# Kernel tuning notes

Measured on AMD Instinct MI355X. Metric: run time of the kernel, lower is better.

Reference implementation:

```python
import jax, jax.numpy as jnp
import numpy as np

B, S, D, H = 4, 2048, 1024, 16
DH = D // H
NEG = -100000.0


def setup_inputs() -> dict:
    key = jax.random.key(0)
    ks = jax.random.split(key, 13)
    s = 1.0 / np.sqrt(D)
    inp = {
        'q': jax.random.normal(ks[0], (B, S, D), jnp.float32),
        'k': jax.random.normal(ks[1], (B, S, D), jnp.float32),
        'v': jax.random.normal(ks[2], (B, S, D), jnp.float32),
        'mask': jax.random.randint(ks[3], (B, 1, S, S), 0, 2).astype(bool),
        'wq_w': jax.random.normal(ks[4], (D, D), jnp.float32) * s,
        'wq_b': jnp.zeros((D,), jnp.float32),
        'wk_w': jax.random.normal(ks[5], (D, D), jnp.float32) * s,
        'wk_b': jnp.zeros((D,), jnp.float32),
        'wv_w': jax.random.normal(ks[6], (D, D), jnp.float32) * s,
        'wv_b': jnp.zeros((D,), jnp.float32),
        'wo_w': jax.random.normal(ks[7], (D, D), jnp.float32) * s,
        'wo_b': jnp.zeros((D,), jnp.float32),
    }
    return inp


def reference(q, k, v, mask, wq_w, wq_b, wk_w, wk_b, wv_w, wv_b, wo_w, wo_b):
    # torch Linear: y = x @ W^T + b
    qh = (q @ wq_w.T + wq_b).reshape(B, S, H, DH).transpose(0, 2, 1, 3)  # [B,H,S,DH]
    kh = (k @ wk_w.T + wk_b).reshape(B, S, H, DH).transpose(0, 2, 1, 3)
    vh = (v @ wv_w.T + wv_b).reshape(B, S, H, DH).transpose(0, 2, 1, 3)
    # NOTE: original code has NO 1/sqrt(d) scaling
    alpha = jnp.einsum('bhqd,bhkd->bhqk', qh, kh)  # [B,H,S,S]
    alpha = jnp.where(mask, NEG, alpha)
    score = jax.nn.softmax(alpha, axis=-1)
    x = jnp.einsum('bhqk,bhkd->bhqd', score, vh)
    x = x.transpose(0, 2, 1, 3).reshape(B, S, D)
    return x @ wo_w.T + wo_b
```

## Files before the change

kernel.cpp:

```cpp
#include <hip/hip_runtime.h>
#include <hip/hip_bf16.h>

#define B_ 4
#define S_ 2048
#define D_ 1024
#define H_ 16
#define NEGV (-100000.0f)

typedef __attribute__((ext_vector_type(8))) short short8;
typedef __attribute__((ext_vector_type(4))) float f32x4;
typedef unsigned short us;

__device__ __forceinline__ us f2h(float f) {
  union { _Float16 h; us u; } c;
  c.h = (_Float16)f;
  return c.u;
}

__global__ void detect_mask_kernel(const int* __restrict__ mi, int* __restrict__ flag) {
  int t = threadIdx.x;
  bool bad = false;
  for (int i = t; i < 16384; i += 64) {
    int v = mi[i];
    bad = bad || (v != 0 && v != 1);
  }
  unsigned long long any = __ballot(bad);
  if (t == 0) flag[0] = (any != 0ull) ? 1 : 0;
}

__global__ __launch_bounds__(256) void pack_mask(const void* __restrict__ maskp,
                                                 const int* __restrict__ flag,
                                                 unsigned* __restrict__ pk) {
  int w = blockIdx.x * 256 + threadIdx.x;
  unsigned bits = 0;
  if (flag[0]) {
    const uint4* p = (const uint4*)((const unsigned char*)maskp + (size_t)w * 32);
#pragma unroll
    for (int q = 0; q < 2; ++q) {
      uint4 v = p[q];
      unsigned vv[4] = {v.x, v.y, v.z, v.w};
#pragma unroll
      for (int e = 0; e < 4; ++e) {
        unsigned byte4 = vv[e];
#pragma unroll
        for (int bb = 0; bb < 4; ++bb)
          bits |= (unsigned)(((byte4 >> (8 * bb)) & 0xffu) != 0) << (q * 16 + e * 4 + bb);
      }
    }
  } else {
    const uint4* p = (const uint4*)((const int*)maskp + (size_t)w * 32);
#pragma unroll
    for (int q = 0; q < 8; ++q) {
      uint4 v = p[q];
      bits |= (unsigned)(v.x != 0) << (q * 4 + 0);
      bits |= (unsigned)(v.y != 0) << (q * 4 + 1);
      bits |= (unsigned)(v.z != 0) << (q * 4 + 2);
      bits |= (unsigned)(v.w != 0) << (q * 4 + 3);
    }
  }
  pk[w] = bits;
}

__global__ __launch_bounds__(256) void cvt_f16(const float* __restrict__ in,
                                               us* __restrict__ out, int n8) {
  int i = blockIdx.x * 256 + threadIdx.x;
  if (i >= n8) return;
  float4 a = ((const float4*)in)[2 * i];
  float4 b = ((const float4*)in)[2 * i + 1];
  us u[8] = {f2h(a.x), f2h(a.y), f2h(a.z), f2h(a.w),
             f2h(b.x), f2h(b.y), f2h(b.z), f2h(b.w)};
  ((uint4*)out)[i] = *(uint4*)u;
}

__global__ __launch_bounds__(256) void cvt_w4(const float* __restrict__ w0,
                                              const float* __restrict__ w1,
                                              const float* __restrict__ w2,
                                              const float* __restrict__ w3,
                                              us* __restrict__ d0, us* __restrict__ d1,
                                              us* __restrict__ d2, us* __restrict__ d3) {
  int which = blockIdx.x >> 9;
  int i = (blockIdx.x & 511) * 256 + threadIdx.x;
  const float* w = which == 0 ? w0 : which == 1 ? w1 : which == 2 ? w2 : w3;
  us* d = which == 0 ? d0 : which == 1 ? d1 : which == 2 ? d2 : d3;
  float4 a = ((const float4*)w)[2 * i];
  float4 b = ((const float4*)w)[2 * i + 1];
  us u[8] = {f2h(a.x), f2h(a.y), f2h(a.z), f2h(a.w),
             f2h(b.x), f2h(b.y), f2h(b.z), f2h(b.w)};
  ((uint4*)d)[i] = *(uint4*)u;
}

__device__ __forceinline__ void gload16(const us* g, us* l) {
  __builtin_amdgcn_global_load_lds((const __attribute__((address_space(1))) void*)g,
                                   (__attribute__((address_space(3))) void*)l, 16, 0, 0);
}

__device__ __forceinline__ int swzb(int row, int c16) {
  return row * 128 + ((c16 ^ (row & 7)) << 4);
}

template <int OMODE>
__global__ __launch_bounds__(256) void gemm_mfma(
    const us* __restrict__ A, const us* __restrict__ W,
    const float* __restrict__ bias, void* __restrict__ Cp, int M, int N, int K) {
  __shared__ __align__(16) us As[2][128 * 64];
  __shared__ __align__(16) us Ws[2][128 * 64];

  const int m0 = blockIdx.x * 128;
  const int n0 = blockIdx.y * 128;
  const int t = threadIdx.x;
  const int w = t >> 6, l = t & 63;
  const int l15 = l & 15, l4 = l >> 4;
  const int wm = w >> 1, wn = w & 1;

  int goff[4];
#pragma unroll
  for (int j = 0; j < 4; ++j) {
    int u = t + j * 256;
    int r = u >> 3, c8 = u & 7;
    int g = c8 ^ (r & 7);
    goff[j] = r * K + g * 8;
  }
  const us* Ag = A + (size_t)m0 * K;
  const us* Wg = W + (size_t)n0 * K;

  f32x4 acc[4][4];
#pragma unroll
  for (int m = 0; m < 4; ++m)
#pragma unroll
    for (int n = 0; n < 4; ++n) acc[m][n] = (f32x4){0.f, 0.f, 0.f, 0.f};

  auto stage = [&](int k0, int bb) {
#pragma unroll
    for (int j = 0; j < 4; ++j) {
      int u = t + j * 256;
      gload16(Ag + goff[j] + k0, &As[bb][u * 8]);
      gload16(Wg + goff[j] + k0, &Ws[bb][u * 8]);
    }
  };

  stage(0, 0);
  __syncthreads();
  int cur = 0;
  for (int k0 = 0; k0 < K; k0 += 64) {
    if (k0 + 64 < K) stage(k0 + 64, cur ^ 1);
#pragma unroll
    for (int ks = 0; ks < 2; ++ks) {
      short8 ah[4], bh_[4];
#pragma unroll
      for (int m = 0; m < 4; ++m)
        ah[m] = *(const short8*)((const char*)As[cur] + swzb(wm * 64 + m * 16 + l15, ks * 4 + l4));
#pragma unroll
      for (int n = 0; n < 4; ++n)
        bh_[n] = *(const short8*)((const char*)Ws[cur] + swzb(wn * 64 + n * 16 + l15, ks * 4 + l4));
#pragma unroll
      for (int m = 0; m < 4; ++m)
#pragma unroll
        for (int n = 0; n < 4; ++n)
          acc[m][n] = __builtin_amdgcn_mfma_f32_16x16x32_f16(ah[m], bh_[n], acc[m][n], 0, 0, 0);
    }
    __syncthreads();
    cur ^= 1;
  }

  float bv[4];
#pragma unroll
  for (int n = 0; n < 4; ++n) bv[n] = bias[n0 + wn * 64 + n * 16 + l15];

#pragma unroll
  for (int m = 0; m < 4; ++m) {
#pragma unroll
    for (int i = 0; i < 4; ++i) {
      int gm = m0 + wm * 64 + m * 16 + l4 * 4 + i;
#pragma unroll
      for (int n = 0; n < 4; ++n) {
        int gn = n0 + wn * 64 + n * 16 + l15;
        float o = acc[m][n][i] + bv[n];
        if constexpr (OMODE == 0) {
          ((float*)Cp)[(size_t)gm * N + gn] = o;
        } else {
          int b = gm >> 11, s = gm & (S_ - 1);
          int hh = gn >> 6, d = gn & 63;
          size_t idx = (((size_t)(b * H_ + hh) << 11) + s) * 64 + d;
          ((us*)Cp)[idx] = f2h(o);
        }
      }
    }
  }
}

__global__ __launch_bounds__(256) void transpose_v(const us* __restrict__ vh,
                                                   us* __restrict__ vt) {
  __shared__ us Ts[64][72];
  int blk = blockIdx.x;
  int bh = blk >> 5, s0 = (blk & 31) << 6;
  int t = threadIdx.x;
#pragma unroll
  for (int p = 0; p < 2; ++p) {
    int c = t + p * 256;
    int rs = c >> 3, c8 = c & 7;
    *(uint4*)&Ts[rs][c8 * 8] = *(const uint4*)(vh + ((size_t)bh * S_ + s0 + rs) * 64 + c8 * 8);
  }
  __syncthreads();
#pragma unroll
  for (int p = 0; p < 2; ++p) {
    int c = t + p * 256;
    int rd = c >> 3, s8 = c & 7;
    union { us u[8]; uint4 v; } tmp;
#pragma unroll
    for (int e = 0; e < 8; ++e) tmp.u[e] = Ts[s8 * 8 + e][rd];
    *(uint4*)(vt + ((size_t)bh * 64 + rd) * S_ + s0 + s8 * 8) = tmp.v;
  }
}

__device__ __forceinline__ int swz(int row, int bc) {
  return (row << 7) + (bc ^ ((row & 7) << 4));
}

__global__ __launch_bounds__(512) void attn_mfma(
    const us* __restrict__ qh, const us* __restrict__ kh,
    const us* __restrict__ vt, const unsigned* __restrict__ pk,
    us* __restrict__ xout) {
  __shared__ __align__(16) us Ks[2][4096];
  __shared__ __align__(16) us Vs[2][4096];
  __shared__ __align__(16) char Ps[16384];

  const int blk = ((blockIdx.x & 7) << 7) + (blockIdx.x >> 3);
  const int bh = blk >> 4;
  const int q0 = (blk & 15) << 7;
  const int b = bh >> 4, h = bh & (H_ - 1);
  const int t = threadIdx.x;
  const int w = t >> 6, l = t & 63;
  const int l15 = l & 15, l4 = l >> 4;

  short8 qf[2];
  {
    const size_t qbase = ((size_t)bh * S_ + q0 + 16 * w + l15) * 64 + l4 * 8;
    qf[0] = *(const short8*)(qh + qbase);
    qf[1] = *(const short8*)(qh + qbase + 32);
  }

  f32x4 accO[4];
#pragma unroll
  for (int jd = 0; jd < 4; ++jd) accO[jd] = (f32x4){0.f, 0.f, 0.f, 0.f};
  float m_i[4], l_p[4];
#pragma unroll
  for (int i = 0; i < 4; ++i) { m_i[i] = -1e30f; l_p[i] = 0.f; }

  const int r_st = t >> 3, c_st = (t & 7) ^ ((t >> 3) & 7);
  const us* kh_src = kh + ((size_t)bh * S_ + r_st) * 64 + c_st * 8;
  const us* vt_src = vt + ((size_t)bh * 64 + r_st) * S_ + c_st * 8;

  auto stage = [&](int k0, int bb) {
    gload16(kh_src + (size_t)k0 * 64, &Ks[bb][t * 8]);
    gload16(vt_src + k0, &Vs[bb][t * 8]);
  };

  stage(0, 0);
  __syncthreads();
  int cur = 0;
  const unsigned* pb = pk + ((size_t)b * S_ + q0 + 16 * w + (l4 << 2)) * (S_ / 32);

  for (int k0 = 0; k0 < S_; k0 += 64) {
    uint2 mw[4];
#pragma unroll
    for (int i = 0; i < 4; ++i) mw[i] = *(const uint2*)(pb + (size_t)i * (S_ / 32) + (k0 >> 5));
    if (k0 + 64 < S_) stage(k0 + 64, cur ^ 1);

    const char* KT = (const char*)Ks[cur];
    const char* VT = (const char*)Vs[cur];

    __builtin_amdgcn_s_setprio(1);
    f32x4 sj[4];
#pragma unroll
    for (int j = 0; j < 4; ++j) {
      f32x4 s = {0.f, 0.f, 0.f, 0.f};
#pragma unroll
      for (int c = 0; c < 2; ++c) {
        short8 kf = *(const short8*)(KT + swz(l15 + 16 * j, l4 * 16 + 64 * c));
        s = __builtin_amdgcn_mfma_f32_16x16x32_f16(qf[c], kf, s, 0, 0, 0);
      }
      sj[j] = s;
    }
    __builtin_amdgcn_s_setprio(0);
#pragma unroll
    for (int j = 0; j < 4; ++j) {
#pragma unroll
      for (int i = 0; i < 4; ++i) {
        unsigned bits = (j < 2) ? mw[i].x : mw[i].y;
        int sh = (l15 + 16 * j) & 31;
        if ((bits >> sh) & 1u) sj[j][i] = NEGV;
      }
    }
    float mx[4];
    bool need = false;
#pragma unroll
    for (int i = 0; i < 4; ++i) {
      float tm = fmaxf(fmaxf(sj[0][i], sj[1][i]), fmaxf(sj[2][i], sj[3][i]));
#pragma unroll
      for (int off = 1; off < 16; off <<= 1) tm = fmaxf(tm, __shfl_xor(tm, off));
      mx[i] = tm;
      need = need || (tm - m_i[i] > 8.0f);
    }
    if (__any(need)) {
#pragma unroll
      for (int i = 0; i < 4; ++i) {
        float mnew = fmaxf(m_i[i], mx[i]);
        float scl = __expf(m_i[i] - mnew);
        l_p[i] *= scl;
#pragma unroll
        for (int jd = 0; jd < 4; ++jd) accO[jd][i] *= scl;
        m_i[i] = mnew;
      }
    }
#pragma unroll
    for (int i = 0; i < 4; ++i) {
      int prow = 16 * w + l4 * 4 + i;
      float p0 = __expf(sj[0][i] - m_i[i]);
      float p1 = __expf(sj[1][i] - m_i[i]);
      float p2 = __expf(sj[2][i] - m_i[i]);
      float p3 = __expf(sj[3][i] - m_i[i]);
      l_p[i] += (p0 + p1) + (p2 + p3);
      unsigned pk01, pk23;
      asm("v_cvt_pkrtz_f16_f32 %0, %1, %2" : "=v"(pk01) : "v"(p0), "v"(p1));
      asm("v_cvt_pkrtz_f16_f32 %0, %1, %2" : "=v"(pk23) : "v"(p2), "v"(p3));
      *(us*)(Ps + swz(prow, l15 * 2)) = (us)pk01;
      *(us*)(Ps + swz(prow, (l15 + 16) * 2)) = (us)(pk01 >> 16);
      *(us*)(Ps + swz(prow, (l15 + 32) * 2)) = (us)pk23;
      *(us*)(Ps + swz(prow, (l15 + 48) * 2)) = (us)(pk23 >> 16);
    }
    asm volatile("s_waitcnt lgkmcnt(0)" ::: "memory");
    __builtin_amdgcn_sched_barrier(0);
    __builtin_amdgcn_s_setprio(1);
#pragma unroll
    for (int kc = 0; kc < 2; ++kc) {
      short8 pa = *(const short8*)(Ps + swz(16 * w + l15, l4 * 16 + 64 * kc));
#pragma unroll
      for (int jd = 0; jd < 4; ++jd) {
        short8 vb = *(const short8*)(VT + swz(l15 + 16 * jd, l4 * 16 + 64 * kc));
        accO[jd] = __builtin_amdgcn_mfma_f32_16x16x32_f16(pa, vb, accO[jd], 0, 0, 0);
      }
    }
    __builtin_amdgcn_s_setprio(0);
    __syncthreads();
    cur ^= 1;
  }

#pragma unroll
  for (int i = 0; i < 4; ++i) {
    float lr = l_p[i];
#pragma unroll
    for (int off = 1; off < 16; off <<= 1) lr += __shfl_xor(lr, off);
    float inv = 1.f / lr;
    int row = q0 + 16 * w + l4 * 4 + i;
    size_t obase = ((size_t)b * S_ + row) * D_ + h * 64 + l15;
#pragma unroll
    for (int jd = 0; jd < 4; ++jd) xout[obase + 16 * jd] = f2h(accO[jd][i] * inv);
  }
}

extern "C" void kernel_launch(void* const* d_in, const int* in_sizes, int n_in,
                              void* d_out, int out_size, void* d_ws, size_t ws_size,
                              hipStream_t stream) {
  const float* q = (const float*)d_in[0];
  const float* k = (const float*)d_in[1];
  const float* v = (const float*)d_in[2];
  const void* mask = d_in[3];
  const float* wq_w = (const float*)d_in[4];
  const float* wq_b = (const float*)d_in[5];
  const float* wk_w = (const float*)d_in[6];
  const float* wk_b = (const float*)d_in[7];
  const float* wv_w = (const float*)d_in[8];
  const float* wv_b = (const float*)d_in[9];
  const float* wo_w = (const float*)d_in[10];
  const float* wo_b = (const float*)d_in[11];

  const size_t NE = (size_t)B_ * S_ * D_;
  const size_t NW = (size_t)D_ * D_;
  char* ws = (char*)d_ws;
  int* flag = (int*)ws;
  unsigned* pk = (unsigned*)(ws + 256);
  us* C0 = (us*)(ws + 256 + (size_t)(B_ * S_ * (S_ / 32)) * 4);
  us* qh = C0 + NE;
  us* kh = qh + NE;
  us* vh = kh + NE;
  us* W0 = vh + NE;
  us* W1 = W0 + NW;
  us* W2 = W1 + NW;
  us* W3 = W2 + NW;

  detect_mask_kernel<<<1, 64, 0, stream>>>((const int*)mask, flag);
  pack_mask<<<(B_ * S_ * (S_ / 32)) / 256, 256, 0, stream>>>(mask, flag, pk);
  cvt_w4<<<2048, 256, 0, stream>>>(wq_w, wk_w, wv_w, wo_w, W0, W1, W2, W3);

  dim3 g(64, 8);
  const int n8 = (int)(NE / 8);

  cvt_f16<<<n8 / 256, 256, 0, stream>>>(q, C0, n8);
  gemm_mfma<2><<<g, 256, 0, stream>>>(C0, W0, wq_b, qh, B_ * S_, D_, D_);

  cvt_f16<<<n8 / 256, 256, 0, stream>>>(k, C0, n8);
  gemm_mfma<2><<<g, 256, 0, stream>>>(C0, W1, wk_b, kh, B_ * S_, D_, D_);

  cvt_f16<<<n8 / 256, 256, 0, stream>>>(v, C0, n8);
  gemm_mfma<2><<<g, 256, 0, stream>>>(C0, W2, wv_b, vh, B_ * S_, D_, D_);

  transpose_v<<<B_ * H_ * (S_ / 64), 256, 0, stream>>>(vh, C0);

  attn_mfma<<<B_ * H_ * (S_ / 128), 512, 0, stream>>>(qh, kh, C0, pk, vh);

  gemm_mfma<0><<<g, 256, 0, stream>>>(vh, W3, wo_b, d_out, B_ * S_, D_, D_);
}
```

Baseline: 404.4 us.

## Batch QKV projections into one launch and transpose S-tile MFMA in attention

The three input conversions and the three QKV projection GEMMs are merged into single launches using blockIdx.z, with a fallback path when workspace is too small. In the attention kernel the QK^T MFMA operands are swapped so each lane holds one query row. This lets softmax max and sum reductions use two cross-lane shuffles instead of per-row 16-lane reductions. Masking becomes branchless via fma, exp uses raw v_exp_f32 with log2e scaling, and P stores are widened to 64-bit. The batched GEMMs need more workspace, and the extra shuffles to rescale accumulator rows add some cost.

```diff
diff --git a/kernel.cpp b/kernel.cpp
--- a/kernel.cpp
+++ b/kernel.cpp
@@ -6,15 +6,22 @@
 #define D_ 1024
 #define H_ 16
 #define NEGV (-100000.0f)
+#define L2E 1.4426950408889634f
 
 typedef __attribute__((ext_vector_type(8))) short short8;
 typedef __attribute__((ext_vector_type(4))) float f32x4;
 typedef unsigned short us;
+typedef unsigned long long u64;
 
 __device__ __forceinline__ us f2h(float f) {
   union { _Float16 h; us u; } c;
   c.h = (_Float16)f;
   return c.u;
+}
+__device__ __forceinline__ float exp2a(float x) {
+  float r;
+  asm("v_exp_f32 %0, %1" : "=v"(r) : "v"(x));
+  return r;
 }
 
 __global__ void detect_mask_kernel(const int* __restrict__ mi, int* __restrict__ flag) {
@@ -61,10 +68,15 @@
   pk[w] = bits;
 }
 
-__global__ __launch_bounds__(256) void cvt_f16(const float* __restrict__ in,
-                                               us* __restrict__ out, int n8) {
-  int i = blockIdx.x * 256 + threadIdx.x;
-  if (i >= n8) return;
+__global__ __launch_bounds__(256) void cvt_f16x3(const float* __restrict__ i0,
+                                                 const float* __restrict__ i1,
+                                                 const float* __restrict__ i2,
+                                                 us* __restrict__ o0, us* __restrict__ o1,
+                                                 us* __restrict__ o2) {
+  int z = blockIdx.x >> 12;
+  int i = (blockIdx.x & 4095) * 256 + threadIdx.x;
+  const float* in = z == 0 ? i0 : z == 1 ? i1 : i2;
+  us* out = z == 0 ? o0 : z == 1 ? o1 : o2;
   float4 a = ((const float4*)in)[2 * i];
   float4 b = ((const float4*)in)[2 * i + 1];
   us u[8] = {f2h(a.x), f2h(a.y), f2h(a.z), f2h(a.w),
@@ -100,10 +112,19 @@
 
 template <int OMODE>
 __global__ __launch_bounds__(256) void gemm_mfma(
-    const us* __restrict__ A, const us* __restrict__ W,
-    const float* __restrict__ bias, void* __restrict__ Cp, int M, int N, int K) {
+    const us* __restrict__ A0, const us* __restrict__ A1, const us* __restrict__ A2,
+    const us* __restrict__ Wp0, const us* __restrict__ Wp1, const us* __restrict__ Wp2,
+    const float* __restrict__ b0, const float* __restrict__ b1, const float* __restrict__ b2,
+    void* __restrict__ C0, void* __restrict__ C1, void* __restrict__ C2,
+    int M, int N, int K) {
   __shared__ __align__(16) us As[2][128 * 64];
   __shared__ __align__(16) us Ws[2][128 * 64];
+
+  const int z = blockIdx.z;
+  const us* A = z == 0 ? A0 : z == 1 ? A1 : A2;
+  const us* W = z == 0 ? Wp0 : z == 1 ? Wp1 : Wp2;
+  const float* bias = z == 0 ? b0 : z == 1 ? b1 : b2;
+  void* Cp = z == 0 ? C0 : z == 1 ? C1 : C2;
 
   const int m0 = blockIdx.x * 128;
   const int n0 = blockIdx.y * 128;
@@ -242,9 +263,7 @@
   f32x4 accO[4];
 #pragma unroll
   for (int jd = 0; jd < 4; ++jd) accO[jd] = (f32x4){0.f, 0.f, 0.f, 0.f};
-  float m_i[4], l_p[4];
-#pragma unroll
-  for (int i = 0; i < 4; ++i) { m_i[i] = -1e30f; l_p[i] = 0.f; }
+  float m_i = -1e30f, l_p = 0.f;
 
   const int r_st = t >> 3, c_st = (t & 7) ^ ((t >> 3) & 7);
   const us* kh_src = kh + ((size_t)bh * S_ + r_st) * 64 + c_st * 8;
@@ -258,12 +277,16 @@
   stage(0, 0);
   __syncthreads();
   int cur = 0;
-  const unsigned* pb = pk + ((size_t)b * S_ + q0 + 16 * w + (l4 << 2)) * (S_ / 32);
+
+  char* Pw = Ps + w * 2048;
+  const int prowb = l15 * 128;
+  const int rr7 = l15 & 7;
+  const int bhalf = l4 >> 1;
+  const int wsub = (l4 & 1) * 8;
+  const unsigned* pb = pk + ((size_t)b * S_ + q0 + 16 * w + l15) * (S_ / 32);
 
   for (int k0 = 0; k0 < S_; k0 += 64) {
-    uint2 mw[4];
-#pragma unroll
-    for (int i = 0; i < 4; ++i) mw[i] = *(const uint2*)(pb + (size_t)i * (S_ / 32) + (k0 >> 5));
+    uint2 mw = *(const uint2*)(pb + (k0 >> 5));
     if (k0 + 64 < S_) stage(k0 + 64, cur ^ 1);
 
     const char* KT = (const char*)Ks[cur];
@@ -277,63 +300,65 @@
 #pragma unroll
       for (int c = 0; c < 2; ++c) {
         short8 kf = *(const short8*)(KT + swz(l15 + 16 * j, l4 * 16 + 64 * c));
-        s = __builtin_amdgcn_mfma_f32_16x16x32_f16(qf[c], kf, s, 0, 0, 0);
+        s = __builtin_amdgcn_mfma_f32_16x16x32_f16(kf, qf[c], s, 0, 0, 0);
       }
       sj[j] = s;
     }
     __builtin_amdgcn_s_setprio(0);
+
+    float tm = -3e38f;
 #pragma unroll
     for (int j = 0; j < 4; ++j) {
+      unsigned wrd = (j < 2) ? mw.x : mw.y;
+      int bb = ((j & 1) << 4) + (l4 << 2);
 #pragma unroll
       for (int i = 0; i < 4; ++i) {
-        unsigned bits = (j < 2) ? mw[i].x : mw[i].y;
-        int sh = (l15 + 16 * j) & 31;
-        if ((bits >> sh) & 1u) sj[j][i] = NEGV;
-      }
-    }
-    float mx[4];
-    bool need = false;
-#pragma unroll
-    for (int i = 0; i < 4; ++i) {
-      float tm = fmaxf(fmaxf(sj[0][i], sj[1][i]), fmaxf(sj[2][i], sj[3][i]));
-#pragma unroll
-      for (int off = 1; off < 16; off <<= 1) tm = fmaxf(tm, __shfl_xor(tm, off));
-      mx[i] = tm;
-      need = need || (tm - m_i[i] > 8.0f);
-    }
-    if (__any(need)) {
-#pragma unroll
-      for (int i = 0; i < 4; ++i) {
-        float mnew = fmaxf(m_i[i], mx[i]);
-        float scl = __expf(m_i[i] - mnew);
-        l_p[i] *= scl;
-#pragma unroll
-        for (int jd = 0; jd < 4; ++jd) accO[jd][i] *= scl;
-        m_i[i] = mnew;
-      }
-    }
-#pragma unroll
-    for (int i = 0; i < 4; ++i) {
-      int prow = 16 * w + l4 * 4 + i;
-      float p0 = __expf(sj[0][i] - m_i[i]);
-      float p1 = __expf(sj[1][i] - m_i[i]);
-      float p2 = __expf(sj[2][i] - m_i[i]);
-      float p3 = __expf(sj[3][i] - m_i[i]);
-      l_p[i] += (p0 + p1) + (p2 + p3);
-      unsigned pk01, pk23;
-      asm("v_cvt_pkrtz_f16_f32 %0, %1, %2" : "=v"(pk01) : "v"(p0), "v"(p1));
-      asm("v_cvt_pkrtz_f16_f32 %0, %1, %2" : "=v"(pk23) : "v"(p2), "v"(p3));
-      *(us*)(Ps + swz(prow, l15 * 2)) = (us)pk01;
-      *(us*)(Ps + swz(prow, (l15 + 16) * 2)) = (us)(pk01 >> 16);
-      *(us*)(Ps + swz(prow, (l15 + 32) * 2)) = (us)pk23;
-      *(us*)(Ps + swz(prow, (l15 + 48) * 2)) = (us)(pk23 >> 16);
+        float bf = (float)((wrd >> (bb + i)) & 1u);
+        sj[j][i] = fmaf(bf, NEGV, sj[j][i]);
+      }
+      tm = fmaxf(tm, fmaxf(fmaxf(sj[j][0], sj[j][1]), fmaxf(sj[j][2], sj[j][3])));
+    }
+    tm = fmaxf(tm, __shfl_xor(tm, 16));
+    tm = fmaxf(tm, __shfl_xor(tm, 32));
+
+    if (__any(tm - m_i > 8.0f)) {
+      float mnew = fmaxf(m_i, tm);
+      float scl = exp2a((m_i - mnew) * L2E);
+      l_p *= scl;
+      m_i = mnew;
+      float sr0 = __shfl(scl, 4 * l4 + 0);
+      float sr1 = __shfl(scl, 4 * l4 + 1);
+      float sr2 = __shfl(scl, 4 * l4 + 2);
+      float sr3 = __shfl(scl, 4 * l4 + 3);
+#pragma unroll
+      for (int jd = 0; jd < 4; ++jd) {
+        accO[jd][0] *= sr0; accO[jd][1] *= sr1;
+        accO[jd][2] *= sr2; accO[jd][3] *= sr3;
+      }
+    }
+
+    float ml2 = m_i * L2E;
+#pragma unroll
+    for (int j = 0; j < 4; ++j) {
+      float p0 = exp2a(fmaf(sj[j][0], L2E, -ml2));
+      float p1 = exp2a(fmaf(sj[j][1], L2E, -ml2));
+      float p2 = exp2a(fmaf(sj[j][2], L2E, -ml2));
+      float p3 = exp2a(fmaf(sj[j][3], L2E, -ml2));
+      l_p += (p0 + p1) + (p2 + p3);
+      unsigned d0, d1;
+      asm("v_cvt_pkrtz_f16_f32 %0, %1, %2" : "=v"(d0) : "v"(p0), "v"(p1));
+      asm("v_cvt_pkrtz_f16_f32 %0, %1, %2" : "=v"(d1) : "v"(p2), "v"(p3));
+      int chunk = ((j << 1) | bhalf) ^ rr7;
+      *(u64*)(Pw + prowb + (chunk << 4) + wsub) = (u64)d0 | ((u64)d1 << 32);
     }
     asm volatile("s_waitcnt lgkmcnt(0)" ::: "memory");
     __builtin_amdgcn_sched_barrier(0);
+
     __builtin_amdgcn_s_setprio(1);
 #pragma unroll
     for (int kc = 0; kc < 2; ++kc) {
-      short8 pa = *(const short8*)(Ps + swz(16 * w + l15, l4 * 16 + 64 * kc));
+      int chR = (4 * kc + l4) ^ rr7;
+      short8 pa = *(const short8*)(Pw + prowb + (chR << 4));
 #pragma unroll
       for (int jd = 0; jd < 4; ++jd) {
         short8 vb = *(const short8*)(VT + swz(l15 + 16 * jd, l4 * 16 + 64 * kc));
@@ -345,16 +370,20 @@
     cur ^= 1;
   }
 
+  float lr = l_p;
+  lr += __shfl_xor(lr, 16);
+  lr += __shfl_xor(lr, 32);
+  float inv0 = 1.f / __shfl(lr, 4 * l4 + 0);
+  float inv1 = 1.f / __shfl(lr, 4 * l4 + 1);
+  float inv2 = 1.f / __shfl(lr, 4 * l4 + 2);
+  float inv3 = 1.f / __shfl(lr, 4 * l4 + 3);
+  float invs[4] = {inv0, inv1, inv2, inv3};
 #pragma unroll
   for (int i = 0; i < 4; ++i) {
-    float lr = l_p[i];
-#pragma unroll
-    for (int off = 1; off < 16; off <<= 1) lr += __shfl_xor(lr, off);
-    float inv = 1.f / lr;
     int row = q0 + 16 * w + l4 * 4 + i;
     size_t obase = ((size_t)b * S_ + row) * D_ + h * 64 + l15;
 #pragma unroll
-    for (int jd = 0; jd < 4; ++jd) xout[obase + 16 * jd] = f2h(accO[jd][i] * inv);
+    for (int jd = 0; jd < 4; ++jd) xout[obase + 16 * jd] = f2h(accO[jd][i] * invs[i]);
   }
 }
 
@@ -376,37 +405,61 @@
 
   const size_t NE = (size_t)B_ * S_ * D_;
   const size_t NW = (size_t)D_ * D_;
+  const size_t PKB = (size_t)(B_ * S_ * (S_ / 32)) * 4;
   char* ws = (char*)d_ws;
   int* flag = (int*)ws;
-  unsigned* pk = (unsigned*)(ws + 256);
-  us* C0 = (us*)(ws + 256 + (size_t)(B_ * S_ * (S_ / 32)) * 4);
-  us* qh = C0 + NE;
-  us* kh = qh + NE;
-  us* vh = kh + NE;
-  us* W0 = vh + NE;
-  us* W1 = W0 + NW;
-  us* W2 = W1 + NW;
-  us* W3 = W2 + NW;
+  unsigned* pkb = (unsigned*)(ws + 256);
+  us* base = (us*)(ws + 256 + PKB);
 
   detect_mask_kernel<<<1, 64, 0, stream>>>((const int*)mask, flag);
-  pack_mask<<<(B_ * S_ * (S_ / 32)) / 256, 256, 0, stream>>>(mask, flag, pk);
-  cvt_w4<<<2048, 256, 0, stream>>>(wq_w, wk_w, wv_w, wo_w, W0, W1, W2, W3);
-
-  dim3 g(64, 8);
-  const int n8 = (int)(NE / 8);
-
-  cvt_f16<<<n8 / 256, 256, 0, stream>>>(q, C0, n8);
-  gemm_mfma<2><<<g, 256, 0, stream>>>(C0, W0, wq_b, qh, B_ * S_, D_, D_);
-
-  cvt_f16<<<n8 / 256, 256, 0, stream>>>(k, C0, n8);
-  gemm_mfma<2><<<g, 256, 0, stream>>>(C0, W1, wk_b, kh, B_ * S_, D_, D_);
-
-  cvt_f16<<<n8 / 256, 256, 0, stream>>>(v, C0, n8);
-  gemm_mfma<2><<<g, 256, 0, stream>>>(C0, W2, wv_b, vh, B_ * S_, D_, D_);
-
-  transpose_v<<<B_ * H_ * (S_ / 64), 256, 0, stream>>>(vh, C0);
-
-  attn_mfma<<<B_ * H_ * (S_ / 128), 512, 0, stream>>>(qh, kh, C0, pk, vh);
-
-  gemm_mfma<0><<<g, 256, 0, stream>>>(vh, W3, wo_b, d_out, B_ * S_, D_, D_);
-}
+  pack_mask<<<2048, 256, 0, stream>>>(mask, flag, pkb);
+
+  dim3 g2(64, 8, 2);
+  dim3 g3(64, 8, 3);
+  dim3 g1(64, 8, 1);
+
+  const size_t fused_need = 256 + PKB + 6 * NE * 2 + 4 * NW * 2;
+  if (ws_size >= fused_need) {
+    us* A0 = base;
+    us* A1 = A0 + NE;
+    us* A2 = A1 + NE;
+    us* A3 = A2 + NE;
+    us* A4 = A3 + NE;
+    us* A5 = A4 + NE;
+    us* W0 = A5 + NE;
+    us* W1 = W0 + NW;
+    us* W2 = W1 + NW;
+    us* W3 = W2 + NW;
+    cvt_w4<<<2048, 256, 0, stream>>>(wq_w, wk_w, wv_w, wo_w, W0, W1, W2, W3);
+    cvt_f16x3<<<3 * 4096, 256, 0, stream>>>(q, k, v, A0, A1, A2);
+    gemm_mfma<2><<<g3, 256, 0, stream>>>(A0, A1, A2, W0, W1, W2, wq_b, wk_b, wv_b,
+                                         A3, A4, A5, B_ * S_, D_, D_);
+    transpose_v<<<2048, 256, 0, stream>>>(A5, A0);
+    attn_mfma<<<1024, 512, 0, stream>>>(A3, A4, A0, pkb, A1);
+    gemm_mfma<0><<<g1, 256, 0, stream>>>(A1, A1, A1, W3, W3, W3, wo_b, wo_b, wo_b,
+                                         d_out, d_out, d_out, B_ * S_, D_, D_);
+  } else {
+    us* A0 = base;
+    us* A1 = A0 + NE;
+    us* A2 = A1 + NE;
+    us* A3 = A2 + NE;
+    us* A4 = A3 + NE;
+    us* W0 = A4 + NE;
+    us* W1 = W0 + NW;
+    us* W2 = W1 + NW;
+    us* W3 = W2 + NW;
+    cvt_w4<<<2048, 256, 0, stream>>>(wq_w, wk_w, wv_w, wo_w, W0, W1, W2, W3);
+    cvt_f16x3<<<2 * 4096, 256, 0, stream>>>(q, k, nullptr, A0, A1, nullptr);
+    gemm_mfma<2><<<g2, 256, 0, stream>>>(A0, A1, nullptr, W0, W1, nullptr, wq_b, wk_b, nullptr,
+                                         A2, A3, nullptr, B_ * S_, D_, D_);
+    cvt_f16x3<<<4096, 256, 0, stream>>>(v, nullptr, nullptr, A0, nullptr, nullptr);
+    gemm_mfma<2><<<g1, 256, 0, stream>>>(A0, nullptr, nullptr, W2, nullptr, nullptr,
+                                         wv_b, nullptr, nullptr, A1, nullptr, nullptr,
+                                         B_ * S_, D_, D_);
+    transpose_v<<<2048, 256, 0, stream>>>(A1, A4);
+    attn_mfma<<<1024, 512, 0, stream>>>(A2, A3, A4, pkb, A0);
+    gemm_mfma<0><<<g1, 256, 0, stream>>>(A0, nullptr, nullptr, W3, nullptr, nullptr,
+                                         wo_b, nullptr, nullptr, d_out, nullptr, nullptr,
+                                         B_ * S_, D_, D_);
+  }
+}
```

Result: faster. 364.1 us (-10.0%).
